# Kernel optimization log

Hardware: AMD Instinct MI355X
Metric: run time of the kernel (lower is better)

## Reference

```python
import jax, jax.numpy as jnp
import numpy as np

T, C, A = 8192, 512, 64  # context_length, embedding_size, attention_size
EPS = 1e-5


def setup_inputs() -> dict:
    key = jax.random.key(0)
    ks = jax.random.split(key, 5)
    x = jax.random.normal(ks[0], (T, C), dtype=jnp.float32)
    x_emb = jax.random.normal(ks[1], (T, C), dtype=jnp.float32)
    Wq = jax.random.normal(ks[2], (C, A), dtype=jnp.float32) / np.sqrt(C)
    Wk = jax.random.normal(ks[3], (C, A), dtype=jnp.float32) / np.sqrt(C)
    Wv = jax.random.normal(ks[4], (C, C), dtype=jnp.float32) / np.sqrt(C)
    return {
        "x": x,
        "x_emb": x_emb,
        "ln_scale": jnp.ones((C,), jnp.float32),
        "ln_bias": jnp.zeros((C,), jnp.float32),
        "Wq": Wq,
        "Wk": Wk,
        "Wv": Wv,
    }


def _layernorm(x, scale, bias):
    mu = jnp.mean(x, axis=-1, keepdims=True)
    var = jnp.mean(jnp.square(x - mu), axis=-1, keepdims=True)
    return (x - mu) * jax.lax.rsqrt(var + EPS) * scale + bias


def reference(x, x_emb, ln_scale, ln_bias, Wq, Wk, Wv):
    t = x.shape[0]
    xx = _layernorm(x, ln_scale, ln_bias)            # [T, C]
    q = xx @ Wq                                       # [T, A]
    k = xx @ Wk                                       # [T, A]
    c = jnp.einsum('ta,sa->ts', q, k) * (A ** -0.5)  # [T, T]
    # causal tril mask; masked positions set to 0 (NO softmax in this module)
    mask = jnp.tril(jnp.ones((t, t), dtype=bool))
    c = jnp.where(mask, c, 0.0)
    v = x_emb @ Wv                                    # [T, C]
    return x + c @ v
```

## Files before the change

kernel.cpp:

```cpp
#include <hip/hip_runtime.h>

#define TT 8192
#define CC 512

typedef unsigned short u16;
typedef unsigned int u32;
typedef __attribute__((ext_vector_type(8))) short bf16x8;
typedef __attribute__((ext_vector_type(4))) float f32x4;

#define VMCNT0() asm volatile("s_waitcnt vmcnt(0)" ::: "memory")
#define LGKM0()  asm volatile("s_waitcnt lgkmcnt(0)" ::: "memory")

__device__ __forceinline__ u16 f2bf(float f) {
    u32 u = __float_as_uint(f);
    return (u16)((u + 0x7FFFu + ((u >> 16) & 1u)) >> 16);
}

__device__ __forceinline__ void gld16(const u16* g, u16* l) {
    __builtin_amdgcn_global_load_lds(
        (const __attribute__((address_space(1))) u32*)g,
        (__attribute__((address_space(3))) u32*)l, 16, 0, 0);
}

__global__ void lnw_kernel(const float* __restrict__ x,
                           const float* __restrict__ scale,
                           const float* __restrict__ bias,
                           const float* __restrict__ Wq,
                           const float* __restrict__ Wk,
                           const float* __restrict__ Wv,
                           const float* __restrict__ xe,
                           u16* __restrict__ xx,
                           u16* __restrict__ wqkt,
                           u16* __restrict__ wvt,
                           u16* __restrict__ xeb) {
    int b = blockIdx.x;
    if (b < 2048) {
        int row = b * 4 + (threadIdx.x >> 6);
        int l = threadIdx.x & 63;
        const float4* xr = (const float4*)(x + (size_t)row * CC);
        float4 a = xr[l * 2], c = xr[l * 2 + 1];
        float s = a.x + a.y + a.z + a.w + c.x + c.y + c.z + c.w;
        float q = a.x*a.x + a.y*a.y + a.z*a.z + a.w*a.w
                + c.x*c.x + c.y*c.y + c.z*c.z + c.w*c.w;
        #pragma unroll
        for (int m = 1; m < 64; m <<= 1) {
            s += __shfl_xor(s, m, 64);
            q += __shfl_xor(q, m, 64);
        }
        float mu = s * (1.0f / CC);
        float var = q * (1.0f / CC) - mu * mu;
        float rs = rsqrtf(var + 1e-5f);
        const float4* sc4 = (const float4*)scale;
        const float4* bi4 = (const float4*)bias;
        float4 s1 = sc4[l * 2], s2 = sc4[l * 2 + 1];
        float4 b1 = bi4[l * 2], b2 = bi4[l * 2 + 1];
        bf16x8 o;
        o[0] = (short)f2bf((a.x - mu) * rs * s1.x + b1.x);
        o[1] = (short)f2bf((a.y - mu) * rs * s1.y + b1.y);
        o[2] = (short)f2bf((a.z - mu) * rs * s1.z + b1.z);
        o[3] = (short)f2bf((a.w - mu) * rs * s1.w + b1.w);
        o[4] = (short)f2bf((c.x - mu) * rs * s2.x + b2.x);
        o[5] = (short)f2bf((c.y - mu) * rs * s2.y + b2.y);
        o[6] = (short)f2bf((c.z - mu) * rs * s2.z + b2.z);
        o[7] = (short)f2bf((c.w - mu) * rs * s2.w + b2.w);
        *(bf16x8*)(xx + (size_t)row * CC + l * 8) = o;
    } else if (b < 3328) {
        int tid = (b - 2048) * 256 + threadIdx.x;
        if (tid < 65536) {
            int c = tid >> 9, k = tid & 511;
            float w = (c < 64) ? Wq[k * 64 + c] * 0.125f : Wk[k * 64 + (c - 64)];
            wqkt[tid] = f2bf(w);
        } else {
            int i = tid - 65536;
            int c = i >> 9, k = i & 511;
            wvt[i] = f2bf(Wv[k * 512 + c]);
        }
    } else {
        size_t i = (size_t)(b - 3328) * 2048 + (size_t)threadIdx.x * 8;
        float4 a = *(const float4*)(xe + i);
        float4 c = *(const float4*)(xe + i + 4);
        bf16x8 o;
        o[0] = (short)f2bf(a.x); o[1] = (short)f2bf(a.y);
        o[2] = (short)f2bf(a.z); o[3] = (short)f2bf(a.w);
        o[4] = (short)f2bf(c.x); o[5] = (short)f2bf(c.y);
        o[6] = (short)f2bf(c.z); o[7] = (short)f2bf(c.w);
        *(bf16x8*)(xeb + i) = o;
    }
}

__global__ __launch_bounds__(512, 4) void qkv_gemm_kernel(const u16* __restrict__ xx,
                                                          const u16* __restrict__ wqkt,
                                                          const u16* __restrict__ xeb,
                                                          const u16* __restrict__ wvt,
                                                          u16* __restrict__ qk,
                                                          u16* __restrict__ kt,
                                                          u16* __restrict__ vt) {
    extern __shared__ u16 smem[];

    const int tid = threadIdx.x;
    const int w = tid >> 6, l = tid & 63;
    const int l15 = l & 15, g = l >> 4;
    const int wr = w >> 2, wc = w & 3;

    const bool isqk = blockIdx.x < 64;
    int r0, c0;
    const u16 *Asrc, *Bsrc;
    if (isqk) { r0 = blockIdx.x * 128; c0 = 0; Asrc = xx; Bsrc = wqkt; }
    else {
        int b2 = blockIdx.x - 64;
        r0 = (b2 >> 2) * 128; c0 = (b2 & 3) * 128; Asrc = xeb; Bsrc = wvt;
    }

    const int drow = tid >> 3, sl = tid & 7;
    #define A_DMA(KK, B) { \
        _Pragma("unroll") \
        for (int i = 0; i < 2; ++i) { \
            int r = i * 64 + drow; \
            gld16(Asrc + (size_t)(r0 + r) * CC + (KK) * 64 + ((sl ^ (r & 7)) << 3), \
                  smem + (B) * 8192 + r * 64 + sl * 8); \
        } }
    #define B_DMA(KK, B) { \
        _Pragma("unroll") \
        for (int i = 0; i < 2; ++i) { \
            int r = i * 64 + drow; \
            gld16(Bsrc + (size_t)(c0 + r) * CC + (KK) * 64 + ((sl ^ (r & 7)) << 3), \
                  smem + 16384 + (B) * 8192 + r * 64 + sl * 8); \
        } }

    f32x4 acc[4][2];
    #pragma unroll
    for (int m = 0; m < 4; ++m)
        #pragma unroll
        for (int n = 0; n < 2; ++n) acc[m][n] = (f32x4){0.f, 0.f, 0.f, 0.f};

    A_DMA(0, 0); B_DMA(0, 0);

    int cur = 0;
    for (int kk = 0; kk < 8; ++kk) {
        VMCNT0();
        LGKM0();
        __builtin_amdgcn_s_barrier();
        if (kk < 7) { A_DMA(kk + 1, cur ^ 1); B_DMA(kk + 1, cur ^ 1); }

        const u16* Ab = smem + cur * 8192;
        const u16* Bb = smem + 16384 + cur * 8192;
        __builtin_amdgcn_s_setprio(1);
        #pragma unroll
        for (int ka = 0; ka < 2; ++ka) {
            bf16x8 af[4], bfr[2];
            #pragma unroll
            for (int Mt = 0; Mt < 4; ++Mt) {
                int r = wr * 64 + Mt * 16 + l15;
                int ph = (ka * 4 + g) ^ (r & 7);
                af[Mt] = *(const bf16x8*)&Ab[r * 64 + ph * 8];
            }
            #pragma unroll
            for (int Nt = 0; Nt < 2; ++Nt) {
                int c = wc * 32 + Nt * 16 + l15;
                int ph = (ka * 4 + g) ^ (c & 7);
                bfr[Nt] = *(const bf16x8*)&Bb[c * 64 + ph * 8];
            }
            #pragma unroll
            for (int Mt = 0; Mt < 4; ++Mt)
                #pragma unroll
                for (int Nt = 0; Nt < 2; ++Nt)
                    acc[Mt][Nt] = __builtin_amdgcn_mfma_f32_16x16x32_bf16(af[Mt], bfr[Nt], acc[Mt][Nt], 0, 0, 0);
        }
        __builtin_amdgcn_s_setprio(0);
        cur ^= 1;
    }

    if (isqk) {
        #pragma unroll
        for (int Mt = 0; Mt < 4; ++Mt) {
            #pragma unroll
            for (int Nt = 0; Nt < 2; ++Nt) {
                int col = wc * 32 + Nt * 16 + l15;
                #pragma unroll
                for (int jj = 0; jj < 4; ++jj) {
                    int row = wr * 64 + Mt * 16 + g * 4 + jj;
                    qk[(size_t)(r0 + row) * 128 + col] = f2bf(acc[Mt][Nt][jj]);
                }
            }
        }
        __syncthreads();
        u16* tl = smem;
        if (wc >= 2) {
            #pragma unroll
            for (int Mt = 0; Mt < 4; ++Mt) {
                #pragma unroll
                for (int Nt = 0; Nt < 2; ++Nt) {
                    int a = (wc - 2) * 32 + Nt * 16 + l15;
                    #pragma unroll
                    for (int jj = 0; jj < 4; ++jj) {
                        int row = wr * 64 + Mt * 16 + g * 4 + jj;
                        tl[a * 136 + row] = f2bf(acc[Mt][Nt][jj]);
                    }
                }
            }
        }
        __syncthreads();
        #pragma unroll
        for (int i = 0; i < 2; ++i) {
            int chunk = i * 512 + tid;
            int a = chunk >> 4, r8 = chunk & 15;
            *(bf16x8*)(kt + (size_t)a * TT + r0 + r8 * 8) = *(const bf16x8*)&tl[a * 136 + r8 * 8];
        }
    } else {
        __syncthreads();
        u16* tl = smem;
        #pragma unroll
        for (int Mt = 0; Mt < 4; ++Mt) {
            #pragma unroll
            for (int Nt = 0; Nt < 2; ++Nt) {
                int col = wc * 32 + Nt * 16 + l15;
                #pragma unroll
                for (int jj = 0; jj < 4; ++jj) {
                    int row = wr * 64 + Mt * 16 + g * 4 + jj;
                    tl[col * 136 + row] = f2bf(acc[Mt][Nt][jj]);
                }
            }
        }
        __syncthreads();
        #pragma unroll
        for (int i = 0; i < 4; ++i) {
            int chunk = i * 512 + tid;
            int c = chunk >> 4, r8 = chunk & 15;
            *(bf16x8*)(vt + (size_t)(c0 + c) * TT + r0 + r8 * 8) = *(const bf16x8*)&tl[c * 136 + r8 * 8];
        }
    }
    #undef A_DMA
    #undef B_DMA
}

__global__ __launch_bounds__(512) void gkv_kernel(const u16* __restrict__ vt,
                                                  const u16* __restrict__ kt,
                                                  float* __restrict__ Gt) {
    int j = blockIdx.x;
    int w = threadIdx.x >> 6, l = threadIdx.x & 63;
    int l15 = l & 15, g = l >> 4;
    int c0 = w * 64;

    f32x4 acc[4][4];
    #pragma unroll
    for (int m = 0; m < 4; ++m)
        #pragma unroll
        for (int n = 0; n < 4; ++n) acc[m][n] = (f32x4){0.f, 0.f, 0.f, 0.f};

    #pragma unroll
    for (int ka = 0; ka < 2; ++ka) {
        int k = j * 64 + ka * 32 + g * 8;
        bf16x8 af[4], bfr[4];
        #pragma unroll
        for (int Mt = 0; Mt < 4; ++Mt)
            af[Mt] = *(const bf16x8*)(vt + (size_t)(c0 + Mt * 16 + l15) * TT + k);
        #pragma unroll
        for (int Nt = 0; Nt < 4; ++Nt)
            bfr[Nt] = *(const bf16x8*)(kt + (size_t)(Nt * 16 + l15) * TT + k);
        #pragma unroll
        for (int Mt = 0; Mt < 4; ++Mt)
            #pragma unroll
            for (int Nt = 0; Nt < 4; ++Nt)
                acc[Mt][Nt] = __builtin_amdgcn_mfma_f32_16x16x32_bf16(af[Mt], bfr[Nt], acc[Mt][Nt], 0, 0, 0);
    }

    float* gp = Gt + (size_t)j * 32768;
    #pragma unroll
    for (int Mt = 0; Mt < 4; ++Mt) {
        #pragma unroll
        for (int Nt = 0; Nt < 4; ++Nt) {
            int a = Nt * 16 + l15;
            #pragma unroll
            for (int jj = 0; jj < 4; ++jj) {
                int c = c0 + Mt * 16 + g * 4 + jj;
                gp[c * 64 + a] = acc[Mt][Nt][jj];
            }
        }
    }
}

__global__ __launch_bounds__(256) void scan_kernel(const float* __restrict__ Gt,
                                                   u16* __restrict__ ptb) {
    int e = blockIdx.x * 256 + threadIdx.x;
    float acc = 0.f;
    ptb[e] = 0;
    for (int i = 1; i < 64; ++i) {
        acc += Gt[(size_t)(2 * i - 2) * 32768 + e] + Gt[(size_t)(2 * i - 1) * 32768 + e];
        ptb[(size_t)i * 32768 + e] = f2bf(acc);
    }
}

__global__ __launch_bounds__(512) void out_kernel(const u16* __restrict__ qk,
                                                  const u16* __restrict__ ptb,
                                                  const u16* __restrict__ vt,
                                                  const float* __restrict__ x,
                                                  float* __restrict__ out) {
    __shared__ u16 Slds[128 * 128];

    const int tid = threadIdx.x;
    const int w = tid >> 6, l = tid & 63;
    const int l15 = l & 15, g = l >> 4;
    const int wr = w >> 2, wcol = w & 3;

    const int rt = (int)blockIdx.x >> 2;
    const int cb = (int)blockIdx.x & 3;

    f32x4 acc[4][2];
    #pragma unroll
    for (int m = 0; m < 4; ++m)
        #pragma unroll
        for (int n = 0; n < 2; ++n) acc[m][n] = (f32x4){0.f, 0.f, 0.f, 0.f};

    const int dq = rt * 128 + w * 16 + l15;
    const bf16x8 qa0 = *(const bf16x8*)(qk + (size_t)dq * 128 + g * 8);
    const bf16x8 qa1 = *(const bf16x8*)(qk + (size_t)dq * 128 + 32 + g * 8);
    #pragma unroll
    for (int Nt = 0; Nt < 8; ++Nt) {
        int scol = Nt * 16 + l15;
        f32x4 sacc = (f32x4){0.f, 0.f, 0.f, 0.f};
        #pragma unroll
        for (int ka = 0; ka < 2; ++ka) {
            bf16x8 kf = *(const bf16x8*)(qk + (size_t)(rt * 128 + scol) * 128 + 64 + ka * 32 + g * 8);
            sacc = __builtin_amdgcn_mfma_f32_16x16x32_bf16(ka ? qa1 : qa0, kf, sacc, 0, 0, 0);
        }
        #pragma unroll
        for (int jj = 0; jj < 4; ++jj) {
            int row = w * 16 + g * 4 + jj;
            float val = (scol > row) ? 0.f : sacc[jj];
            int slot = (scol >> 3) ^ (row & 15);
            Slds[row * 128 + slot * 8 + (scol & 7)] = f2bf(val);
        }
    }

    #pragma unroll
    for (int ka = 0; ka < 2; ++ka) {
        bf16x8 qf[4], pf[2];
        #pragma unroll
        for (int Mt = 0; Mt < 4; ++Mt)
            qf[Mt] = *(const bf16x8*)(qk + (size_t)(rt * 128 + wr * 64 + Mt * 16 + l15) * 128 + ka * 32 + g * 8);
        #pragma unroll
        for (int Nt = 0; Nt < 2; ++Nt) {
            int c = cb * 128 + wcol * 32 + Nt * 16 + l15;
            pf[Nt] = *(const bf16x8*)(ptb + (size_t)rt * 32768 + c * 64 + ka * 32 + g * 8);
        }
        #pragma unroll
        for (int Mt = 0; Mt < 4; ++Mt)
            #pragma unroll
            for (int Nt = 0; Nt < 2; ++Nt)
                acc[Mt][Nt] = __builtin_amdgcn_mfma_f32_16x16x32_bf16(qf[Mt], pf[Nt], acc[Mt][Nt], 0, 0, 0);
    }

    __syncthreads();

    #pragma unroll
    for (int ks = 0; ks < 4; ++ks) {
        bf16x8 sf[4], vf[2];
        #pragma unroll
        for (int Mt = 0; Mt < 4; ++Mt) {
            int row = wr * 64 + Mt * 16 + l15;
            int slot = (ks * 4 + g) ^ (row & 15);
            sf[Mt] = *(const bf16x8*)&Slds[row * 128 + slot * 8];
        }
        #pragma unroll
        for (int Nt = 0; Nt < 2; ++Nt) {
            int c = cb * 128 + wcol * 32 + Nt * 16 + l15;
            vf[Nt] = *(const bf16x8*)(vt + (size_t)c * TT + rt * 128 + ks * 32 + g * 8);
        }
        #pragma unroll
        for (int Mt = 0; Mt < 4; ++Mt)
            #pragma unroll
            for (int Nt = 0; Nt < 2; ++Nt)
                acc[Mt][Nt] = __builtin_amdgcn_mfma_f32_16x16x32_bf16(sf[Mt], vf[Nt], acc[Mt][Nt], 0, 0, 0);
    }

    #pragma unroll
    for (int Mt = 0; Mt < 4; ++Mt) {
        #pragma unroll
        for (int Nt = 0; Nt < 2; ++Nt) {
            int col = cb * 128 + wcol * 32 + Nt * 16 + l15;
            #pragma unroll
            for (int jj = 0; jj < 4; ++jj) {
                int row = rt * 128 + wr * 64 + Mt * 16 + g * 4 + jj;
                out[(size_t)row * 512 + col] = x[(size_t)row * 512 + col] + acc[Mt][Nt][jj];
            }
        }
    }
}

extern "C" void kernel_launch(void* const* d_in, const int* in_sizes, int n_in,
                              void* d_out, int out_size, void* d_ws, size_t ws_size,
                              hipStream_t stream) {
    (void)in_sizes; (void)n_in; (void)out_size; (void)ws_size;
    const float* x    = (const float*)d_in[0];
    const float* xe   = (const float*)d_in[1];
    const float* lns  = (const float*)d_in[2];
    const float* lnb  = (const float*)d_in[3];
    const float* Wq   = (const float*)d_in[4];
    const float* Wk   = (const float*)d_in[5];
    const float* Wv   = (const float*)d_in[6];
    float* out = (float*)d_out;
    char* ws = (char*)d_ws;

    size_t off_xx   = 0;
    size_t off_qk   = off_xx   + (size_t)TT * CC * 2;
    size_t off_wqkt = off_qk   + (size_t)TT * 128 * 2;
    size_t off_wvt  = off_wqkt + (size_t)128 * 512 * 2;
    size_t off_vt   = off_wvt  + (size_t)512 * 512 * 2;
    size_t off_xeb  = off_vt   + (size_t)TT * CC * 2;
    size_t off_kt   = off_xeb  + (size_t)TT * CC * 2;
    size_t off_gt   = off_kt   + (size_t)64 * TT * 2;
    size_t off_ptb  = off_gt   + (size_t)128 * 32768 * 4;

    u16* xx   = (u16*)(ws + off_xx);
    u16* qk   = (u16*)(ws + off_qk);
    u16* wqkt = (u16*)(ws + off_wqkt);
    u16* wvt  = (u16*)(ws + off_wvt);
    u16* vt   = (u16*)(ws + off_vt);
    u16* xeb  = (u16*)(ws + off_xeb);
    u16* kt   = (u16*)(ws + off_kt);
    float* Gt = (float*)(ws + off_gt);
    u16* ptb  = (u16*)(ws + off_ptb);

    const size_t qkv_lds = 65536;

    hipLaunchKernelGGL(lnw_kernel,      dim3(5376), dim3(256), 0, stream,
                       x, lns, lnb, Wq, Wk, Wv, xe, xx, wqkt, wvt, xeb);
    hipLaunchKernelGGL(qkv_gemm_kernel, dim3(320),  dim3(512), qkv_lds, stream,
                       xx, wqkt, xeb, wvt, qk, kt, vt);
    hipLaunchKernelGGL(gkv_kernel,      dim3(128),  dim3(512), 0, stream, vt, kt, Gt);
    hipLaunchKernelGGL(scan_kernel,     dim3(128),  dim3(256), 0, stream, Gt, ptb);
    hipLaunchKernelGGL(out_kernel,      dim3(256),  dim3(512), 0, stream, qk, ptb, vt, x, out);
}
```

Baseline: 62.79 us.

## Use 128-row chunk states and a two-level parallel prefix scan

```diff
diff --git a/kernel.cpp b/kernel.cpp
--- a/kernel.cpp
+++ b/kernel.cpp
@@ -235,58 +235,73 @@
 
 __global__ __launch_bounds__(512) void gkv_kernel(const u16* __restrict__ vt,
                                                   const u16* __restrict__ kt,
-                                                  float* __restrict__ Gt) {
-    int j = blockIdx.x;
+                                                  float* __restrict__ H) {
+    int m = blockIdx.x >> 2, cq = blockIdx.x & 3;
     int w = threadIdx.x >> 6, l = threadIdx.x & 63;
     int l15 = l & 15, g = l >> 4;
-    int c0 = w * 64;
-
-    f32x4 acc[4][4];
-    #pragma unroll
-    for (int m = 0; m < 4; ++m)
-        #pragma unroll
-        for (int n = 0; n < 4; ++n) acc[m][n] = (f32x4){0.f, 0.f, 0.f, 0.f};
-
-    #pragma unroll
-    for (int ka = 0; ka < 2; ++ka) {
-        int k = j * 64 + ka * 32 + g * 8;
-        bf16x8 af[4], bfr[4];
-        #pragma unroll
-        for (int Mt = 0; Mt < 4; ++Mt)
+    int c0 = cq * 128 + (w >> 1) * 32;
+    int a0 = (w & 1) * 32;
+
+    f32x4 acc[2][2];
+    #pragma unroll
+    for (int i = 0; i < 2; ++i)
+        #pragma unroll
+        for (int n = 0; n < 2; ++n) acc[i][n] = (f32x4){0.f, 0.f, 0.f, 0.f};
+
+    #pragma unroll
+    for (int ka = 0; ka < 4; ++ka) {
+        int k = m * 128 + ka * 32 + g * 8;
+        bf16x8 af[2], bfr[2];
+        #pragma unroll
+        for (int Mt = 0; Mt < 2; ++Mt)
             af[Mt] = *(const bf16x8*)(vt + (size_t)(c0 + Mt * 16 + l15) * TT + k);
         #pragma unroll
-        for (int Nt = 0; Nt < 4; ++Nt)
-            bfr[Nt] = *(const bf16x8*)(kt + (size_t)(Nt * 16 + l15) * TT + k);
-        #pragma unroll
-        for (int Mt = 0; Mt < 4; ++Mt)
-            #pragma unroll
-            for (int Nt = 0; Nt < 4; ++Nt)
+        for (int Nt = 0; Nt < 2; ++Nt)
+            bfr[Nt] = *(const bf16x8*)(kt + (size_t)(a0 + Nt * 16 + l15) * TT + k);
+        #pragma unroll
+        for (int Mt = 0; Mt < 2; ++Mt)
+            #pragma unroll
+            for (int Nt = 0; Nt < 2; ++Nt)
                 acc[Mt][Nt] = __builtin_amdgcn_mfma_f32_16x16x32_bf16(af[Mt], bfr[Nt], acc[Mt][Nt], 0, 0, 0);
     }
 
-    float* gp = Gt + (size_t)j * 32768;
-    #pragma unroll
-    for (int Mt = 0; Mt < 4; ++Mt) {
-        #pragma unroll
-        for (int Nt = 0; Nt < 4; ++Nt) {
-            int a = Nt * 16 + l15;
+    float* hp = H + (size_t)m * 32768;
+    #pragma unroll
+    for (int Mt = 0; Mt < 2; ++Mt) {
+        #pragma unroll
+        for (int Nt = 0; Nt < 2; ++Nt) {
+            int a = a0 + Nt * 16 + l15;
             #pragma unroll
             for (int jj = 0; jj < 4; ++jj) {
                 int c = c0 + Mt * 16 + g * 4 + jj;
-                gp[c * 64 + a] = acc[Mt][Nt][jj];
-            }
-        }
-    }
-}
-
-__global__ __launch_bounds__(256) void scan_kernel(const float* __restrict__ Gt,
-                                                   u16* __restrict__ ptb) {
-    int e = blockIdx.x * 256 + threadIdx.x;
+                hp[c * 64 + a] = acc[Mt][Nt][jj];
+            }
+        }
+    }
+}
+
+__global__ __launch_bounds__(256) void scanA_kernel(const float* __restrict__ H,
+                                                    float* __restrict__ Asum) {
+    int idx = blockIdx.x * 256 + threadIdx.x;
+    int g = idx >> 15, e = idx & 32767;
+    float s = 0.f;
+    #pragma unroll
+    for (int t = 0; t < 8; ++t) s += H[(size_t)(8 * g + t) * 32768 + e];
+    Asum[(size_t)g * 32768 + e] = s;
+}
+
+__global__ __launch_bounds__(256) void scanB_kernel(const float* __restrict__ H,
+                                                    const float* __restrict__ Asum,
+                                                    u16* __restrict__ ptb) {
+    int idx = blockIdx.x * 256 + threadIdx.x;
+    int g = idx >> 15, e = idx & 32767;
     float acc = 0.f;
-    ptb[e] = 0;
-    for (int i = 1; i < 64; ++i) {
-        acc += Gt[(size_t)(2 * i - 2) * 32768 + e] + Gt[(size_t)(2 * i - 1) * 32768 + e];
-        ptb[(size_t)i * 32768 + e] = f2bf(acc);
+    for (int g2 = 0; g2 < g; ++g2) acc += Asum[(size_t)g2 * 32768 + e];
+    ptb[(size_t)(8 * g) * 32768 + e] = f2bf(acc);
+    #pragma unroll
+    for (int t = 1; t < 8; ++t) {
+        acc += H[(size_t)(8 * g + t - 1) * 32768 + e];
+        ptb[(size_t)(8 * g + t) * 32768 + e] = f2bf(acc);
     }
 }
 
@@ -408,8 +423,9 @@
     size_t off_vt   = off_wvt  + (size_t)512 * 512 * 2;
     size_t off_xeb  = off_vt   + (size_t)TT * CC * 2;
     size_t off_kt   = off_xeb  + (size_t)TT * CC * 2;
-    size_t off_gt   = off_kt   + (size_t)64 * TT * 2;
-    size_t off_ptb  = off_gt   + (size_t)128 * 32768 * 4;
+    size_t off_h    = off_kt   + (size_t)64 * TT * 2;
+    size_t off_as   = off_h    + (size_t)64 * 32768 * 4;
+    size_t off_ptb  = off_as   + (size_t)8 * 32768 * 4;
 
     u16* xx   = (u16*)(ws + off_xx);
     u16* qk   = (u16*)(ws + off_qk);
@@ -418,7 +434,8 @@
     u16* vt   = (u16*)(ws + off_vt);
     u16* xeb  = (u16*)(ws + off_xeb);
     u16* kt   = (u16*)(ws + off_kt);
-    float* Gt = (float*)(ws + off_gt);
+    float* H  = (float*)(ws + off_h);
+    float* As = (float*)(ws + off_as);
     u16* ptb  = (u16*)(ws + off_ptb);
 
     const size_t qkv_lds = 65536;
@@ -427,7 +444,8 @@
                        x, lns, lnb, Wq, Wk, Wv, xe, xx, wqkt, wvt, xeb);
     hipLaunchKernelGGL(qkv_gemm_kernel, dim3(320),  dim3(512), qkv_lds, stream,
                        xx, wqkt, xeb, wvt, qk, kt, vt);
-    hipLaunchKernelGGL(gkv_kernel,      dim3(128),  dim3(512), 0, stream, vt, kt, Gt);
-    hipLaunchKernelGGL(scan_kernel,     dim3(128),  dim3(256), 0, stream, Gt, ptb);
+    hipLaunchKernelGGL(gkv_kernel,      dim3(256),  dim3(512), 0, stream, vt, kt, H);
+    hipLaunchKernelGGL(scanA_kernel,    dim3(1024), dim3(256), 0, stream, H, As);
+    hipLaunchKernelGGL(scanB_kernel,    dim3(1024), dim3(256), 0, stream, H, As, ptb);
     hipLaunchKernelGGL(out_kernel,      dim3(256),  dim3(512), 0, stream, qk, ptb, vt, x, out);
 }
```

Measured after the change: 54.29 us, median of 2. 13.5% less time.
